# Kernel tuning notes

Measured on AMD Instinct MI355X. Metric: run time of the kernel, lower is better.

The kernel has to match this reference:

```python
import jax, jax.numpy as jnp
import numpy as np

# Closed-form water-filling solution of the CvxpyLayer problem:
#   maximize  x @ w + sum(entr(w))   s.t.  sum(w) == 1,  w <= c  (w >= 0 via entr domain)
# KKT:  w_i = min(c, exp(x_i - nu))  with nu s.t. sum_i w_i = 1 (monotone in nu -> bisection).

N_SAMPLES = 32768
N_ASSETS = 512
MAX_WEIGHT = 0.02   # init kwarg max_weight
BISECT_ITERS = 60   # ~fp32 precision on nu


def setup_inputs() -> dict:
    key = jax.random.key(0)
    x = jax.random.normal(key, (N_SAMPLES, N_ASSETS), dtype=jnp.float32)
    return {"x": x}


def _entropic_waterfill(x, c):
    # Bisection on the dual variable nu, vectorized over the batch. shapes: x [B,N]
    lo = jnp.min(x, axis=-1, keepdims=True) - 40.0  # all weights at cap -> sum = N*c > 1
    hi = jnp.max(x, axis=-1, keepdims=True) + 40.0  # all weights ~ e^-40 -> sum < 1

    def body(i, carry):
        lo, hi = carry
        mid = 0.5 * (lo + hi)
        s = jnp.sum(jnp.minimum(c, jnp.exp(x - mid)), axis=-1, keepdims=True)
        too_big = s > 1.0
        return jnp.where(too_big, mid, lo), jnp.where(too_big, hi, mid)

    lo, hi = jax.lax.fori_loop(0, BISECT_ITERS, body, (lo, hi))
    nu0 = jax.lax.stop_gradient(0.5 * (lo + hi))

    # Fix the active set (constants w.r.t. x), then express nu in closed form so that
    # plain autodiff yields the exact implicit-function gradients:
    #   sum_{i inactive} exp(x_i - nu) = 1 - c*|active|  =>  nu = logsumexp_inactive(x) - log(r)
    active = jax.lax.stop_gradient(jnp.exp(x - nu0) >= c)          # [B,N] bool
    r = 1.0 - c * jnp.sum(active, axis=-1, keepdims=True)           # residual mass, > 0
    x_inact = jnp.where(active, -jnp.inf, x)
    nu = jax.nn.logsumexp(x_inact, axis=-1, keepdims=True) - jnp.log(r)
    w = jnp.where(active, c, jnp.exp(x - nu))                       # [B,N], sums to 1
    return w


def reference(x):
    return _entropic_waterfill(x, MAX_WEIGHT)
```

## Files before the change

kernel.cpp:

```cpp
#include <hip/hip_runtime.h>


#define N_ASSETS 512
#define C_CAP 0.02f
#define ROWS_PER_BLOCK 4

__global__ __launch_bounds__(256, 4) void waterfill_kernel(
    const float* __restrict__ x, float* __restrict__ out, int n_rows) {
  const int wave = threadIdx.x >> 6;
  const int lane = threadIdx.x & 63;
  const int row = blockIdx.x * ROWS_PER_BLOCK + wave;
  if (row >= n_rows) return;

  const float* xr = x + (size_t)row * N_ASSETS;
  float* wr = out + (size_t)row * N_ASSETS;

  float4 a = reinterpret_cast<const float4*>(xr)[lane];
  float4 b = reinterpret_cast<const float4*>(xr)[lane + 64];

  float e[8];
  e[0] = __expf(a.x); e[1] = __expf(a.y); e[2] = __expf(a.z); e[3] = __expf(a.w);
  e[4] = __expf(b.x); e[5] = __expf(b.y); e[6] = __expf(b.z); e[7] = __expf(b.w);

  float S = ((e[0] + e[1]) + (e[2] + e[3])) + ((e[4] + e[5]) + (e[6] + e[7]));
#pragma unroll
  for (int m = 1; m < 64; m <<= 1) S += __shfl_xor(S, m, 64);

  float u = 1.0f / S;
  int kprev = -1;
  for (int it = 0; it < 50; ++it) {
    const float th = C_CAP / u;
    float s_act = 0.0f, cnt = 0.0f;
#pragma unroll
    for (int j = 0; j < 8; ++j) {
      const bool act = e[j] >= th;
      s_act += act ? e[j] : 0.0f;
      cnt += act ? 1.0f : 0.0f;
    }
#pragma unroll
    for (int m = 1; m < 64; m <<= 1) {
      s_act += __shfl_xor(s_act, m, 64);
      cnt += __shfl_xor(cnt, m, 64);
    }
    const int k = (int)cnt;
    const float r = fmaxf(1.0f - C_CAP * cnt, 1e-12f);
    const float Sin = fmaxf(S - s_act, 1e-30f);
    u = r / Sin;
    if (k == kprev) break;
    kprev = k;
  }

  float4 oa, ob;
  oa.x = fminf(C_CAP, e[0] * u);
  oa.y = fminf(C_CAP, e[1] * u);
  oa.z = fminf(C_CAP, e[2] * u);
  oa.w = fminf(C_CAP, e[3] * u);
  ob.x = fminf(C_CAP, e[4] * u);
  ob.y = fminf(C_CAP, e[5] * u);
  ob.z = fminf(C_CAP, e[6] * u);
  ob.w = fminf(C_CAP, e[7] * u);
  reinterpret_cast<float4*>(wr)[lane] = oa;
  reinterpret_cast<float4*>(wr)[lane + 64] = ob;
}

extern "C" void kernel_launch(void* const* d_in, const int* in_sizes, int n_in,
                              void* d_out, int out_size, void* d_ws, size_t ws_size,
                              hipStream_t stream) {
  const float* x = (const float*)d_in[0];
  float* out = (float*)d_out;
  const int n_rows = in_sizes[0] / N_ASSETS;
  const int grid = (n_rows + ROWS_PER_BLOCK - 1) / ROWS_PER_BLOCK;
  waterfill_kernel<<<grid, 256, 0, stream>>>(x, out, n_rows);
}
```

Baseline: 25.33 us.

## Process two rows per wave and count active set via ballot popcount

Each wave now handles two rows (r and r+half), interleaving their fixed-point iterations to hide shuffle latency and halve the grid. Active-set counts use ballot+popcount instead of a float shuffle reduction, and the masked-sum reduction is skipped once the count stops changing. The iteration cap drops from 50 to 16. Odd row counts would leave the last row unprocessed, and higher register use per wave may reduce occupancy.

```diff
diff --git a/kernel.cpp b/kernel.cpp
--- a/kernel.cpp
+++ b/kernel.cpp
@@ -3,64 +3,94 @@
 
 #define N_ASSETS 512
 #define C_CAP 0.02f
-#define ROWS_PER_BLOCK 4
 
-__global__ __launch_bounds__(256, 4) void waterfill_kernel(
-    const float* __restrict__ x, float* __restrict__ out, int n_rows) {
+__device__ __forceinline__ float wave_sum(float v) {
+#pragma unroll
+  for (int m = 1; m < 64; m <<= 1) v += __shfl_xor(v, m, 64);
+  return v;
+}
+
+__global__ __launch_bounds__(256) void waterfill_kernel(
+    const float* __restrict__ x, float* __restrict__ out, int half) {
   const int wave = threadIdx.x >> 6;
   const int lane = threadIdx.x & 63;
-  const int row = blockIdx.x * ROWS_PER_BLOCK + wave;
-  if (row >= n_rows) return;
+  const int r0 = blockIdx.x * 4 + wave;
+  if (r0 >= half) return;
+  const size_t off0 = (size_t)r0 * N_ASSETS;
+  const size_t off1 = (size_t)(r0 + half) * N_ASSETS;
 
-  const float* xr = x + (size_t)row * N_ASSETS;
-  float* wr = out + (size_t)row * N_ASSETS;
+  const float4* xa = reinterpret_cast<const float4*>(x + off0);
+  const float4* xb = reinterpret_cast<const float4*>(x + off1);
+  float4 A0 = xa[lane], A1 = xa[lane + 64];
+  float4 B0 = xb[lane], B1 = xb[lane + 64];
 
-  float4 a = reinterpret_cast<const float4*>(xr)[lane];
-  float4 b = reinterpret_cast<const float4*>(xr)[lane + 64];
+  float ea[8], eb[8];
+  ea[0] = __expf(A0.x); ea[1] = __expf(A0.y); ea[2] = __expf(A0.z); ea[3] = __expf(A0.w);
+  ea[4] = __expf(A1.x); ea[5] = __expf(A1.y); ea[6] = __expf(A1.z); ea[7] = __expf(A1.w);
+  eb[0] = __expf(B0.x); eb[1] = __expf(B0.y); eb[2] = __expf(B0.z); eb[3] = __expf(B0.w);
+  eb[4] = __expf(B1.x); eb[5] = __expf(B1.y); eb[6] = __expf(B1.z); eb[7] = __expf(B1.w);
 
-  float e[8];
-  e[0] = __expf(a.x); e[1] = __expf(a.y); e[2] = __expf(a.z); e[3] = __expf(a.w);
-  e[4] = __expf(b.x); e[5] = __expf(b.y); e[6] = __expf(b.z); e[7] = __expf(b.w);
-
-  float S = ((e[0] + e[1]) + (e[2] + e[3])) + ((e[4] + e[5]) + (e[6] + e[7]));
+  float sa = ((ea[0] + ea[1]) + (ea[2] + ea[3])) + ((ea[4] + ea[5]) + (ea[6] + ea[7]));
+  float sb = ((eb[0] + eb[1]) + (eb[2] + eb[3])) + ((eb[4] + eb[5]) + (eb[6] + eb[7]));
 #pragma unroll
-  for (int m = 1; m < 64; m <<= 1) S += __shfl_xor(S, m, 64);
-
-  float u = 1.0f / S;
-  int kprev = -1;
-  for (int it = 0; it < 50; ++it) {
-    const float th = C_CAP / u;
-    float s_act = 0.0f, cnt = 0.0f;
-#pragma unroll
-    for (int j = 0; j < 8; ++j) {
-      const bool act = e[j] >= th;
-      s_act += act ? e[j] : 0.0f;
-      cnt += act ? 1.0f : 0.0f;
-    }
-#pragma unroll
-    for (int m = 1; m < 64; m <<= 1) {
-      s_act += __shfl_xor(s_act, m, 64);
-      cnt += __shfl_xor(cnt, m, 64);
-    }
-    const int k = (int)cnt;
-    const float r = fmaxf(1.0f - C_CAP * cnt, 1e-12f);
-    const float Sin = fmaxf(S - s_act, 1e-30f);
-    u = r / Sin;
-    if (k == kprev) break;
-    kprev = k;
+  for (int m = 1; m < 64; m <<= 1) {
+    sa += __shfl_xor(sa, m, 64);
+    sb += __shfl_xor(sb, m, 64);
   }
 
-  float4 oa, ob;
-  oa.x = fminf(C_CAP, e[0] * u);
-  oa.y = fminf(C_CAP, e[1] * u);
-  oa.z = fminf(C_CAP, e[2] * u);
-  oa.w = fminf(C_CAP, e[3] * u);
-  ob.x = fminf(C_CAP, e[4] * u);
-  ob.y = fminf(C_CAP, e[5] * u);
-  ob.z = fminf(C_CAP, e[6] * u);
-  ob.w = fminf(C_CAP, e[7] * u);
-  reinterpret_cast<float4*>(wr)[lane] = oa;
-  reinterpret_cast<float4*>(wr)[lane + 64] = ob;
+  float ua = 1.0f / sa, ub = 1.0f / sb;
+  int ka_prev = 0, kb_prev = 0;
+  bool done_a = false, done_b = false;
+  for (int it = 0; it < 16 && !(done_a && done_b); ++it) {
+    if (!done_a) {
+      const float th = C_CAP / ua;
+      int k = 0;
+#pragma unroll
+      for (int j = 0; j < 8; ++j) k += (int)__popcll(__ballot(ea[j] >= th));
+      if (k == ka_prev) {
+        done_a = true;
+      } else {
+        float s = 0.0f;
+#pragma unroll
+        for (int j = 0; j < 8; ++j) s += (ea[j] >= th) ? ea[j] : 0.0f;
+        s = wave_sum(s);
+        ua = fmaxf(1.0f - C_CAP * (float)k, 1e-12f) / fmaxf(sa - s, 1e-30f);
+        ka_prev = k;
+      }
+    }
+    if (!done_b) {
+      const float th = C_CAP / ub;
+      int k = 0;
+#pragma unroll
+      for (int j = 0; j < 8; ++j) k += (int)__popcll(__ballot(eb[j] >= th));
+      if (k == kb_prev) {
+        done_b = true;
+      } else {
+        float s = 0.0f;
+#pragma unroll
+        for (int j = 0; j < 8; ++j) s += (eb[j] >= th) ? eb[j] : 0.0f;
+        s = wave_sum(s);
+        ub = fmaxf(1.0f - C_CAP * (float)k, 1e-12f) / fmaxf(sb - s, 1e-30f);
+        kb_prev = k;
+      }
+    }
+  }
+
+  float* wa = out + off0;
+  float* wb = out + off1;
+  float4 oa0, oa1, ob0, ob1;
+  oa0.x = fminf(C_CAP, ea[0] * ua); oa0.y = fminf(C_CAP, ea[1] * ua);
+  oa0.z = fminf(C_CAP, ea[2] * ua); oa0.w = fminf(C_CAP, ea[3] * ua);
+  oa1.x = fminf(C_CAP, ea[4] * ua); oa1.y = fminf(C_CAP, ea[5] * ua);
+  oa1.z = fminf(C_CAP, ea[6] * ua); oa1.w = fminf(C_CAP, ea[7] * ua);
+  ob0.x = fminf(C_CAP, eb[0] * ub); ob0.y = fminf(C_CAP, eb[1] * ub);
+  ob0.z = fminf(C_CAP, eb[2] * ub); ob0.w = fminf(C_CAP, eb[3] * ub);
+  ob1.x = fminf(C_CAP, eb[4] * ub); ob1.y = fminf(C_CAP, eb[5] * ub);
+  ob1.z = fminf(C_CAP, eb[6] * ub); ob1.w = fminf(C_CAP, eb[7] * ub);
+  reinterpret_cast<float4*>(wa)[lane] = oa0;
+  reinterpret_cast<float4*>(wa)[lane + 64] = oa1;
+  reinterpret_cast<float4*>(wb)[lane] = ob0;
+  reinterpret_cast<float4*>(wb)[lane + 64] = ob1;
 }
 
 extern "C" void kernel_launch(void* const* d_in, const int* in_sizes, int n_in,
@@ -69,6 +99,7 @@
   const float* x = (const float*)d_in[0];
   float* out = (float*)d_out;
   const int n_rows = in_sizes[0] / N_ASSETS;
-  const int grid = (n_rows + ROWS_PER_BLOCK - 1) / ROWS_PER_BLOCK;
-  waterfill_kernel<<<grid, 256, 0, stream>>>(x, out, n_rows);
+  const int half = n_rows >> 1;
+  const int grid = (half + 3) / 4;
+  waterfill_kernel<<<grid, 256, 0, stream>>>(x, out, half);
 }
```

Result: no change. 25.64 us (+1.2%).
